# Optimization experiments

Hardware: AMD Instinct MI355X
Metric: run time of the kernel (lower is better)

The kernel has to match this reference:

```python
import jax, jax.numpy as jnp
import numpy as np

LAM = 0.9
ALPHA = 1.0
EPS = 1e-8

def _get_weight(prob):
    # prob: [N, C]; if 1-D it would be stacked with 1-prob (not the case here)
    if prob.ndim == 1:
        prob = jnp.stack([prob, 1.0 - prob], axis=1)
    top2 = jax.lax.top_k(prob, 2)[0]  # [N, 2], sorted descending
    fir, sec = top2[:, 0], top2[:, 1]
    # exp(alpha * (lam*log(fir+eps) + (1-lam)*log(fir-sec+eps)))
    return jnp.exp(ALPHA * (LAM * jnp.log(fir + EPS) + (1.0 - LAM) * jnp.log(fir - sec + EPS)))

def setup_inputs() -> dict:
    key = jax.random.key(0)
    k1, k2, k3, k4 = jax.random.split(key, 4)
    N, D, C = 500000, 128, 10
    v1 = jax.random.normal(k1, (N, D), dtype=jnp.float32)
    v2 = jax.random.normal(k2, (N, D), dtype=jnp.float32)
    prob_v1 = jax.random.uniform(k3, (N, C), dtype=jnp.float32)
    prob_v2 = jax.random.uniform(k4, (N, C), dtype=jnp.float32)
    return {"v1": v1, "prob_v1": prob_v1, "v2": v2, "prob_v2": prob_v2}

def reference(v1, prob_v1, v2, prob_v2):
    w1 = _get_weight(prob_v1)  # [N]
    w2 = _get_weight(prob_v2)  # [N]
    denom = w1 + w2
    beta1 = (w1 / denom)[:, None]  # [N, 1]
    beta2 = (w2 / denom)[:, None]
    # name='cora' branch: row-wise broadcast fuse (dense math; torch returns .to_sparse() of this)
    return beta1 * v1 + beta2 * v2
```

## Files before the change

### kernel.cpp

```cpp
#include <hip/hip_runtime.h>
#include <math.h>

#define LAM 0.9f
#define EPS 1e-8f
#define ROWS_PER_BLOCK 256

typedef float  f32x4 __attribute__((ext_vector_type(4)));
typedef float  f32x2 __attribute__((ext_vector_type(2)));

__device__ __forceinline__ float row_logw(const float* __restrict__ p) {
    float fir = -3.4e38f, sec = -3.4e38f;
    const f32x2* p2 = (const f32x2*)p;
#pragma unroll
    for (int i = 0; i < 5; ++i) {
        f32x2 x = p2[i];
        if (x.x > fir) { sec = fir; fir = x.x; }
        else if (x.x > sec) { sec = x.x; }
        if (x.y > fir) { sec = fir; fir = x.y; }
        else if (x.y > sec) { sec = x.y; }
    }
    return LAM * __logf(fir + EPS) + (1.0f - LAM) * __logf(fir - sec + EPS);
}

__global__ __launch_bounds__(256) void fused_blend_kernel(
    const float* __restrict__ v1, const float* __restrict__ p1,
    const float* __restrict__ v2, const float* __restrict__ p2,
    float* __restrict__ out, int N)
{
    __shared__ float b1s[ROWS_PER_BLOCK];

    const int t = threadIdx.x;
    const int rowBase = blockIdx.x * ROWS_PER_BLOCK;
    const int row = rowBase + t;

    if (row < N) {
        const float a1 = row_logw(p1 + (size_t)row * 10);
        const float a2 = row_logw(p2 + (size_t)row * 10);
        b1s[t] = 1.0f / (1.0f + __expf(a2 - a1));
    }
    __syncthreads();

    const unsigned gEnd  = (unsigned)N * 32u;
    const unsigned gBase = (unsigned)rowBase * 32u;
    const f32x4* __restrict__ v1q = (const f32x4*)v1;
    const f32x4* __restrict__ v2q = (const f32x4*)v2;
    f32x4* __restrict__ outq = (f32x4*)out;
#pragma unroll 8
    for (int k = 0; k < 32; ++k) {
        const unsigned g = gBase + (unsigned)k * 256u + (unsigned)t;
        if (g < gEnd) {
            const int localRow = (k * 256 + t) >> 5;
            const float beta1 = b1s[localRow];
            const float beta2 = 1.0f - beta1;
            const f32x4 va = v1q[g];
            const f32x4 vb = v2q[g];
            f32x4 r = beta1 * va + beta2 * vb;
            __builtin_nontemporal_store(r, outq + g);
        }
    }
}

extern "C" void kernel_launch(void* const* d_in, const int* in_sizes, int n_in,
                              void* d_out, int out_size, void* d_ws, size_t ws_size,
                              hipStream_t stream) {
    const float* v1 = (const float*)d_in[0];
    const float* p1 = (const float*)d_in[1];
    const float* v2 = (const float*)d_in[2];
    const float* p2 = (const float*)d_in[3];
    float* out = (float*)d_out;
    const int N = in_sizes[1] / 10;

    const int blocks = (N + ROWS_PER_BLOCK - 1) / ROWS_PER_BLOCK;
    fused_blend_kernel<<<blocks, 256, 0, stream>>>(v1, p1, v2, p2, out, N);
}
```

Baseline: 164.6 us.

## Prefetch v1/v2 before weight computation and double-buffer loads in registers

For full blocks, the kernel now issues the first 8 vector loads of v1 and v2 before computing the per-row weights and the barrier, so memory latency overlaps the top-2/log math. The remaining chunks are software-pipelined with two register buffers, loading the next 8 while blending and storing the previous ones. Out-of-range checks are dropped on full blocks, and a separate guarded path handles the tail block. This raises register pressure (64 f32x4 live values), which may lower occupancy.

New measurement: 153.0 us. 7.0% less time.

```diff
diff --git a/kernel.cpp b/kernel.cpp
--- a/kernel.cpp
+++ b/kernel.cpp
@@ -3,10 +3,10 @@
 
 #define LAM 0.9f
 #define EPS 1e-8f
-#define ROWS_PER_BLOCK 256
+#define RPB 256
 
-typedef float  f32x4 __attribute__((ext_vector_type(4)));
-typedef float  f32x2 __attribute__((ext_vector_type(2)));
+typedef float f32x4 __attribute__((ext_vector_type(4)));
+typedef float f32x2 __attribute__((ext_vector_type(2)));
 
 __device__ __forceinline__ float row_logw(const float* __restrict__ p) {
     float fir = -3.4e38f, sec = -3.4e38f;
@@ -27,35 +27,88 @@
     const float* __restrict__ v2, const float* __restrict__ p2,
     float* __restrict__ out, int N)
 {
-    __shared__ float b1s[ROWS_PER_BLOCK];
+    __shared__ float b1s[RPB];
+    const int t   = threadIdx.x;
+    const int t32 = t >> 5;
+    const int rowBase = blockIdx.x * RPB;
+    const int row = rowBase + t;
+    const unsigned gBase = (unsigned)rowBase * 32u + (unsigned)t;
 
-    const int t = threadIdx.x;
-    const int rowBase = blockIdx.x * ROWS_PER_BLOCK;
-    const int row = rowBase + t;
+    const f32x4* __restrict__ v1q = (const f32x4*)v1;
+    const f32x4* __restrict__ v2q = (const f32x4*)v2;
+    f32x4* __restrict__ outq = (f32x4*)out;
 
-    if (row < N) {
+    const bool full = (rowBase + RPB <= N);
+
+    if (full) {
+        f32x4 aA[8], bA[8], aB[8], bB[8];
+
+#pragma unroll
+        for (int j = 0; j < 8; ++j) {
+            aA[j] = v1q[gBase + (unsigned)j * 256u];
+            bA[j] = v2q[gBase + (unsigned)j * 256u];
+        }
+
         const float a1 = row_logw(p1 + (size_t)row * 10);
         const float a2 = row_logw(p2 + (size_t)row * 10);
         b1s[t] = 1.0f / (1.0f + __expf(a2 - a1));
-    }
-    __syncthreads();
+        __syncthreads();
 
-    const unsigned gEnd  = (unsigned)N * 32u;
-    const unsigned gBase = (unsigned)rowBase * 32u;
-    const f32x4* __restrict__ v1q = (const f32x4*)v1;
-    const f32x4* __restrict__ v2q = (const f32x4*)v2;
-    f32x4* __restrict__ outq = (f32x4*)out;
-#pragma unroll 8
-    for (int k = 0; k < 32; ++k) {
-        const unsigned g = gBase + (unsigned)k * 256u + (unsigned)t;
-        if (g < gEnd) {
-            const int localRow = (k * 256 + t) >> 5;
-            const float beta1 = b1s[localRow];
-            const float beta2 = 1.0f - beta1;
-            const f32x4 va = v1q[g];
-            const f32x4 vb = v2q[g];
-            f32x4 r = beta1 * va + beta2 * vb;
-            __builtin_nontemporal_store(r, outq + g);
+#pragma unroll
+        for (int j = 0; j < 8; ++j) {
+            aB[j] = v1q[gBase + (unsigned)(8 + j) * 256u];
+            bB[j] = v2q[gBase + (unsigned)(8 + j) * 256u];
+        }
+#pragma unroll
+        for (int j = 0; j < 8; ++j) {
+            const float be1 = b1s[j * 8 + t32];
+            __builtin_nontemporal_store(be1 * aA[j] + (1.0f - be1) * bA[j],
+                                        outq + gBase + (unsigned)j * 256u);
+        }
+#pragma unroll
+        for (int j = 0; j < 8; ++j) {
+            aA[j] = v1q[gBase + (unsigned)(16 + j) * 256u];
+            bA[j] = v2q[gBase + (unsigned)(16 + j) * 256u];
+        }
+#pragma unroll
+        for (int j = 0; j < 8; ++j) {
+            const float be1 = b1s[(8 + j) * 8 + t32];
+            __builtin_nontemporal_store(be1 * aB[j] + (1.0f - be1) * bB[j],
+                                        outq + gBase + (unsigned)(8 + j) * 256u);
+        }
+#pragma unroll
+        for (int j = 0; j < 8; ++j) {
+            aB[j] = v1q[gBase + (unsigned)(24 + j) * 256u];
+            bB[j] = v2q[gBase + (unsigned)(24 + j) * 256u];
+        }
+#pragma unroll
+        for (int j = 0; j < 8; ++j) {
+            const float be1 = b1s[(16 + j) * 8 + t32];
+            __builtin_nontemporal_store(be1 * aA[j] + (1.0f - be1) * bA[j],
+                                        outq + gBase + (unsigned)(16 + j) * 256u);
+        }
+#pragma unroll
+        for (int j = 0; j < 8; ++j) {
+            const float be1 = b1s[(24 + j) * 8 + t32];
+            __builtin_nontemporal_store(be1 * aB[j] + (1.0f - be1) * bB[j],
+                                        outq + gBase + (unsigned)(24 + j) * 256u);
+        }
+    } else {
+        if (row < N) {
+            const float a1 = row_logw(p1 + (size_t)row * 10);
+            const float a2 = row_logw(p2 + (size_t)row * 10);
+            b1s[t] = 1.0f / (1.0f + __expf(a2 - a1));
+        }
+        __syncthreads();
+        const unsigned gEnd = (unsigned)N * 32u;
+        for (int k = 0; k < 32; ++k) {
+            const unsigned g = (unsigned)rowBase * 32u + (unsigned)k * 256u + (unsigned)t;
+            if (g < gEnd) {
+                const float be1 = b1s[(k * 256 + t) >> 5];
+                const f32x4 va = v1q[g];
+                const f32x4 vb = v2q[g];
+                __builtin_nontemporal_store(be1 * va + (1.0f - be1) * vb, outq + g);
+            }
         }
     }
 }
@@ -70,6 +123,6 @@
     float* out = (float*)d_out;
     const int N = in_sizes[1] / 10;
 
-    const int blocks = (N + ROWS_PER_BLOCK - 1) / ROWS_PER_BLOCK;
+    const int blocks = (N + RPB - 1) / RPB;
     fused_blend_kernel<<<blocks, 256, 0, stream>>>(v1, p1, v2, p2, out, N);
 }
```
